# Optimization experiments

Measured on AMD Instinct MI355X. Metric: run time of the kernel, lower is better.

The kernel has to match this reference:

```python
import jax, jax.numpy as jnp
import numpy as np

K = 8192
D = 256


def setup_inputs() -> dict:
    key = jax.random.key(0)
    k1, k2 = jax.random.split(key)
    z_e_x = jax.random.normal(k1, (8, D, 1024), dtype=jnp.float32)  # (B, D, T)
    # nn.Embedding(K, D) weight init: uniform(-1/K, 1/K)
    codebook = jax.random.uniform(k2, (K, D), dtype=jnp.float32,
                                  minval=-1.0 / K, maxval=1.0 / K)
    return {"z_e_x": z_e_x, "codebook": codebook}


def reference(z_e_x, codebook):
    # z_e_x: (B, D, T) -> (B, T, D), matching z_e_x.permute(0, 2, 1)
    z = jnp.transpose(z_e_x, (0, 2, 1))  # (B, T, D)
    # squared L2 distance: ||z||^2 + ||e||^2 - 2 z @ e^T
    z_sq = jnp.sum(z * z, axis=-1, keepdims=True)            # (B, T, 1)
    e_sq = jnp.sum(codebook * codebook, axis=-1)             # (K,)
    cross = jnp.einsum('btd,kd->btk', z, codebook)           # (B, T, K)
    dists = z_sq + e_sq[None, None, :] - 2.0 * cross         # (B, T, K)
    indices = jnp.argmin(dists, axis=-1)                     # (B, T) int
    return indices
```

## Files before the change

kernel.cpp:

```cpp
#include <hip/hip_runtime.h>
#include <cfloat>
#include <stdint.h>

#define KC 8192
#define NQ 8192
#define DD 256
#define NSTAGE 8

typedef _Float16 f16;
typedef _Float16 half8 __attribute__((ext_vector_type(8)));
typedef float floatx4 __attribute__((ext_vector_type(4)));

#define WS_AH   0
#define WS_AL   4194304
#define WS_BH   8388608
#define WS_BL1  12582912
#define WS_KEY1 16777216
#define WS_NEED1 (16777216ull + 65536ull)
#define WS_BL2  10485760
#define WS_KEY2 12582912

__device__ __forceinline__ void prep_b_body(const float* __restrict__ cb,
                                            f16* __restrict__ Bh, f16* __restrict__ Bl,
                                            int kofs, int gid) {
    int n = gid & 127;
    int q = (gid >> 7) & 3;
    int s = (gid >> 9) & 7;
    int ntl = gid >> 12;
    int K = kofs + ntl * 128 + n;
    int d0 = s * 32 + q * 8;
    const float4 v0 = *(const float4*)(cb + (size_t)K * DD + d0);
    const float4 v1 = *(const float4*)(cb + (size_t)K * DD + d0 + 4);
    float vv[8] = {v0.x, v0.y, v0.z, v0.w, v1.x, v1.y, v1.z, v1.w};
    half8 eh8, el8;
    #pragma unroll
    for (int j = 0; j < 8; ++j) {
        float e = vv[j] * 8192.0f;
        f16 h = (f16)e;
        eh8[j] = h;
        el8[j] = (f16)(e - (float)h);
    }
    *(half8*)(Bh + (size_t)gid * 8) = eh8;
    *(half8*)(Bl + (size_t)gid * 8) = el8;
}

__device__ __forceinline__ void prep_a_vec_body(const float* __restrict__ z,
                                                f16* __restrict__ Ah, f16* __restrict__ Al,
                                                int bid, int tid) {
    const int mt = bid >> 3;
    const int s  = bid & 7;
    const int q  = tid >> 6;
    const int lane = tid & 63;
    const int r0 = lane * 4;
    const int Q0 = mt * 256;
    const int b = Q0 >> 10;
    const int t0 = (Q0 & 1023) + r0;
    const float* zp = z + (size_t)b * (DD * 1024) + t0;
    const int d0 = s * 32 + q * 8;
    float4 v[8];
    #pragma unroll
    for (int j = 0; j < 8; ++j)
        v[j] = *(const float4*)(zp + (size_t)(d0 + j) * 1024);
    const size_t gbase = (((size_t)(mt * 8 + s) * 4 + q) * 256 + r0);
    #pragma unroll
    for (int dq = 0; dq < 4; ++dq) {
        half8 zh8, zl8;
        #pragma unroll
        for (int j = 0; j < 8; ++j) {
            float vv = (dq == 0) ? v[j].x : (dq == 1) ? v[j].y : (dq == 2) ? v[j].z : v[j].w;
            f16 h = (f16)vv;
            zh8[j] = h;
            zl8[j] = (f16)(vv - (float)h);
        }
        *(half8*)(Ah + (gbase + dq) * 8) = zh8;
        *(half8*)(Al + (gbase + dq) * 8) = zl8;
    }
}

__device__ __forceinline__ void zsq2_body(const float* __restrict__ z,
                                          float* __restrict__ zsq,
                                          unsigned long long* __restrict__ key,
                                          int gid) {
    int q = gid >> 1, half = gid & 1;
    int b = q >> 10, t = q & 1023;
    const float* p = z + (size_t)b * (DD * 1024) + t + (size_t)(half * 128) * 1024;
    float s = 0.f;
    #pragma unroll 8
    for (int d = 0; d < 128; ++d) { float v = p[(size_t)d * 1024]; s = fmaf(v, v, s); }
    float so = __shfl_xor(s, 1, 64);
    if (half == 0) { zsq[q] = s + so; key[q] = ~0ull; }
}

__global__ void vq_prep_all(const float* __restrict__ z, const float* __restrict__ cb,
                            f16* __restrict__ Ah, f16* __restrict__ Al,
                            f16* __restrict__ Bh, f16* __restrict__ Bl,
                            float* __restrict__ zsq, unsigned long long* __restrict__ key) {
    int bid = blockIdx.x;
    int tid = threadIdx.x;
    if (bid < 64) {
        zsq2_body(z, zsq, key, bid * 256 + tid);
    } else if (bid < 320) {
        prep_a_vec_body(z, Ah, Al, bid - 64, tid);
    } else {
        prep_b_body(cb, Bh, Bl, 0, (bid - 320) * 256 + tid);
    }
}

__global__ void vq_prep_az(const float* __restrict__ z,
                           f16* __restrict__ Ah, f16* __restrict__ Al,
                           float* __restrict__ zsq, unsigned long long* __restrict__ key) {
    int bid = blockIdx.x;
    if (bid < 64) zsq2_body(z, zsq, key, bid * 256 + threadIdx.x);
    else          prep_a_vec_body(z, Ah, Al, bid - 64, threadIdx.x);
}
__global__ void vq_prep_b(const float* __restrict__ cb,
                          f16* __restrict__ Bh, f16* __restrict__ Bl, int kofs) {
    prep_b_body(cb, Bh, Bl, kofs, blockIdx.x * 256 + threadIdx.x);
}

__global__ __launch_bounds__(256, 4)
void vq_gemm16(const f16* __restrict__ Ah, const f16* __restrict__ Al,
               const f16* __restrict__ Bh, const f16* __restrict__ Bl,
               const float* __restrict__ zsq, unsigned long long* __restrict__ keyp,
               int kofs) {
    const int flat = blockIdx.x;
    const int xcd = flat & 7;
    const int idx = flat >> 3;
    const int mh2 = xcd * 8 + ((idx >> 3) & 7);
    const int ntl = (idx >> 6) * 8 + (idx & 7);
    const int tid = threadIdx.x;
    const int lane = tid & 63;
    const int wv = tid >> 6;
    const int wm = wv >> 1, wn = wv & 1;
    const int quad = lane >> 4;
    const int l16 = lane & 15;

    __shared__ unsigned long long kbuf[256];

    floatx4 acc[4][4];
    #pragma unroll
    for (int i = 0; i < 4; ++i)
        #pragma unroll
        for (int j = 0; j < 4; ++j) acc[i][j] = (floatx4)0.f;

    const int mt = mh2 >> 1;
    const int r0 = (mh2 & 1) * 128;
    const size_t abase = ((((size_t)(mt * 8) * 4) + quad) * 256
                          + (size_t)(r0 + wm * 64 + l16)) * 8;
    const f16* Ap  = Ah + abase;
    const f16* Alp = Al + abase;
    const f16* Bpb = Bh + ((size_t)(ntl * 8) * 4 + quad) * 1024 + (size_t)(wn * 64 + l16) * 8;
    const f16* Blb = Bl + ((size_t)(ntl * 8) * 4 + quad) * 1024 + (size_t)(wn * 64 + l16) * 8;

    for (int s = 0; s < NSTAGE; ++s) {
        half8 bhf[4], blf[4];
        #pragma unroll
        for (int nj = 0; nj < 4; ++nj) {
            bhf[nj] = *(const half8*)(Bpb + nj * 128);
            blf[nj] = *(const half8*)(Blb + nj * 128);
        }
        half8 av[4], aw[4];
        #pragma unroll
        for (int mi = 0; mi < 4; ++mi) {
            av[mi] = *(const half8*)(Ap  + (size_t)mi * 128);
            aw[mi] = *(const half8*)(Alp + (size_t)mi * 128);
        }
        #pragma unroll
        for (int mi = 0; mi < 4; ++mi)
            #pragma unroll
            for (int nj = 0; nj < 4; ++nj)
                acc[mi][nj] = __builtin_amdgcn_mfma_f32_16x16x32_f16(av[mi], bhf[nj], acc[mi][nj], 0, 0, 0);
        #pragma unroll
        for (int mi = 0; mi < 4; ++mi)
            #pragma unroll
            for (int nj = 0; nj < 4; ++nj)
                acc[mi][nj] = __builtin_amdgcn_mfma_f32_16x16x32_f16(av[mi], blf[nj], acc[mi][nj], 0, 0, 0);
        #pragma unroll
        for (int mi = 0; mi < 4; ++mi)
            #pragma unroll
            for (int nj = 0; nj < 4; ++nj)
                acc[mi][nj] = __builtin_amdgcn_mfma_f32_16x16x32_f16(aw[mi], bhf[nj], acc[mi][nj], 0, 0, 0);
        Ap  += 8192; Alp += 8192;
        Bpb += 4096; Blb += 4096;
    }

    const int kb = kofs + ntl * 128 + wn * 64;
    #pragma unroll
    for (int mi = 0; mi < 4; ++mi) {
        #pragma unroll
        for (int reg = 0; reg < 4; ++reg) {
            int qlocal = wm * 64 + mi * 16 + quad * 4 + reg;
            float zq = zsq[mh2 * 128 + qlocal];
            float bd = FLT_MAX; int bk = 0;
            #pragma unroll
            for (int nj = 0; nj < 4; ++nj) {
                float dd = zq - acc[mi][nj][reg] * 0x1p-12f;
                int kk = kb + nj * 16 + l16;
                if (dd < bd || (dd == bd && kk < bk)) { bd = dd; bk = kk; }
            }
            #pragma unroll
            for (int mm = 1; mm <= 8; mm <<= 1) {
                float od = __shfl_xor(bd, mm, 64);
                int ok = __shfl_xor(bk, mm, 64);
                if (od < bd || (od == bd && ok < bk)) { bd = od; bk = ok; }
            }
            if (l16 == 0)
                kbuf[wn * 128 + qlocal] =
                    ((unsigned long long)__float_as_uint(bd) << 32) | (unsigned int)bk;
        }
    }
    __syncthreads();
    if (tid < 128) {
        unsigned long long k0 = kbuf[tid];
        unsigned long long k1 = kbuf[128 + tid];
        unsigned long long key = (k1 < k0) ? k1 : k0;
        atomicMin(&keyp[mh2 * 128 + tid], key);
    }
}

__global__ void vq_extract(const unsigned long long* __restrict__ key,
                           int* __restrict__ out) {
    int q = blockIdx.x * 256 + threadIdx.x;
    out[q] = (int)(key[q] & 0xFFFFFFFFull);
}

extern "C" void kernel_launch(void* const* d_in, const int* in_sizes, int n_in,
                              void* d_out, int out_size, void* d_ws, size_t ws_size,
                              hipStream_t stream) {
    const float* z  = (const float*)d_in[0];
    const float* cb = (const float*)d_in[1];
    char* ws = (char*)d_ws;
    f16* Ah = (f16*)(ws + WS_AH);
    f16* Al = (f16*)(ws + WS_AL);
    float* zsq = (float*)d_out;
    int* out = (int*)d_out;

    if (ws_size >= WS_NEED1) {
        f16* Bh = (f16*)(ws + WS_BH);
        f16* Bl = (f16*)(ws + WS_BL1);
        unsigned long long* key = (unsigned long long*)(ws + WS_KEY1);
        vq_prep_all<<<1344, 256, 0, stream>>>(z, cb, Ah, Al, Bh, Bl, zsq, key);
        vq_gemm16<<<4096, 256, 0, stream>>>(Ah, Al, Bh, Bl, zsq, key, 0);
        vq_extract<<<NQ / 256, 256, 0, stream>>>(key, out);
    } else {
        f16* Bh = (f16*)(ws + WS_BH);
        f16* Bl = (f16*)(ws + WS_BL2);
        unsigned long long* key = (unsigned long long*)(ws + WS_KEY2);
        vq_prep_az<<<320, 256, 0, stream>>>(z, Ah, Al, zsq, key);
        for (int p = 0; p < 2; ++p) {
            int kofs = p * 4096;
            vq_prep_b<<<512, 256, 0, stream>>>(cb, Bh, Bl, kofs);
            vq_gemm16<<<2048, 256, 0, stream>>>(Ah, Al, Bh, Bl, zsq, key, kofs);
        }
        vq_extract<<<NQ / 256, 256, 0, stream>>>(key, out);
    }
}
```

Before: 187.9 us.

## Switch GEMM from 16x16x32 to 32x32x16 MFMA with matching operand layout

Replaces the 16x16x32 f16 MFMA tiling (4x4 accumulators per wave) with 32x32x16 MFMA (2x2 floatx16 accumulators). The A and B prep kernels now write a permuted K-chunk layout so each half-wave loads contiguous half8 fragments in the order the 32x32 instruction expects. The epilogue argmin reduction is reworked for the 32-lane output pattern. The aim is higher MFMA throughput and fewer operand loads per FLOP. The risk is a layout or index mismatch, since the permutation, pointer strides and row mapping must all agree.

```diff
diff --git a/kernel.cpp b/kernel.cpp
--- a/kernel.cpp
+++ b/kernel.cpp
@@ -9,7 +9,7 @@
 
 typedef _Float16 f16;
 typedef _Float16 half8 __attribute__((ext_vector_type(8)));
-typedef float floatx4 __attribute__((ext_vector_type(4)));
+typedef float floatx16 __attribute__((ext_vector_type(16)));
 
 #define WS_AH   0
 #define WS_AL   4194304
@@ -40,8 +40,10 @@
         eh8[j] = h;
         el8[j] = (f16)(e - (float)h);
     }
-    *(half8*)(Bh + (size_t)gid * 8) = eh8;
-    *(half8*)(Bl + (size_t)gid * 8) = el8;
+    int sig = ((q & 1) << 1) | (q >> 1);
+    size_t og = ((size_t)(ntl * 8 + s) * 4 + sig) * 128 + n;
+    *(half8*)(Bh + og * 8) = eh8;
+    *(half8*)(Bl + og * 8) = el8;
 }
 
 __device__ __forceinline__ void prep_a_vec_body(const float* __restrict__ z,
@@ -61,7 +63,9 @@
     #pragma unroll
     for (int j = 0; j < 8; ++j)
         v[j] = *(const float4*)(zp + (size_t)(d0 + j) * 1024);
-    const size_t gbase = (((size_t)(mt * 8 + s) * 4 + q) * 256 + r0);
+    const int sig = ((q & 1) << 1) | (q >> 1);
+    const int mh2 = mt * 2 + (r0 >> 7);
+    const size_t gbase = ((size_t)(mh2 * 8 + s) * 4 + sig) * 128 + (r0 & 127);
     #pragma unroll
     for (int dq = 0; dq < 4; ++dq) {
         half8 zh8, zl8;
@@ -119,7 +123,7 @@
 }
 
 __global__ __launch_bounds__(256, 4)
-void vq_gemm16(const f16* __restrict__ Ah, const f16* __restrict__ Al,
+void vq_gemm32(const f16* __restrict__ Ah, const f16* __restrict__ Al,
                const f16* __restrict__ Bh, const f16* __restrict__ Bl,
                const float* __restrict__ zsq, unsigned long long* __restrict__ keyp,
                int kofs) {
@@ -132,79 +136,85 @@
     const int lane = tid & 63;
     const int wv = tid >> 6;
     const int wm = wv >> 1, wn = wv & 1;
-    const int quad = lane >> 4;
-    const int l16 = lane & 15;
+    const int hi = lane >> 5;
+    const int l32 = lane & 31;
 
     __shared__ unsigned long long kbuf[256];
 
-    floatx4 acc[4][4];
-    #pragma unroll
-    for (int i = 0; i < 4; ++i)
-        #pragma unroll
-        for (int j = 0; j < 4; ++j) acc[i][j] = (floatx4)0.f;
-
-    const int mt = mh2 >> 1;
-    const int r0 = (mh2 & 1) * 128;
-    const size_t abase = ((((size_t)(mt * 8) * 4) + quad) * 256
-                          + (size_t)(r0 + wm * 64 + l16)) * 8;
-    const f16* Ap  = Ah + abase;
-    const f16* Alp = Al + abase;
-    const f16* Bpb = Bh + ((size_t)(ntl * 8) * 4 + quad) * 1024 + (size_t)(wn * 64 + l16) * 8;
-    const f16* Blb = Bl + ((size_t)(ntl * 8) * 4 + quad) * 1024 + (size_t)(wn * 64 + l16) * 8;
+    floatx16 acc[2][2];
+    #pragma unroll
+    for (int i = 0; i < 2; ++i)
+        #pragma unroll
+        for (int j = 0; j < 2; ++j) acc[i][j] = (floatx16)0.f;
+
+    const f16* Ap  = Ah + ((size_t)(mh2 * 32 + 2 * hi)) * 1024
+                        + (size_t)(wm * 64 + l32) * 8;
+    const f16* Alp = Al + ((size_t)(mh2 * 32 + 2 * hi)) * 1024
+                        + (size_t)(wm * 64 + l32) * 8;
+    const f16* Bpb = Bh + ((size_t)(ntl * 32 + 2 * hi)) * 1024
+                        + (size_t)(wn * 64 + l32) * 8;
+    const f16* Blb = Bl + ((size_t)(ntl * 32 + 2 * hi)) * 1024
+                        + (size_t)(wn * 64 + l32) * 8;
 
     for (int s = 0; s < NSTAGE; ++s) {
-        half8 bhf[4], blf[4];
-        #pragma unroll
-        for (int nj = 0; nj < 4; ++nj) {
-            bhf[nj] = *(const half8*)(Bpb + nj * 128);
-            blf[nj] = *(const half8*)(Blb + nj * 128);
-        }
-        half8 av[4], aw[4];
-        #pragma unroll
-        for (int mi = 0; mi < 4; ++mi) {
-            av[mi] = *(const half8*)(Ap  + (size_t)mi * 128);
-            aw[mi] = *(const half8*)(Alp + (size_t)mi * 128);
-        }
-        #pragma unroll
-        for (int mi = 0; mi < 4; ++mi)
-            #pragma unroll
-            for (int nj = 0; nj < 4; ++nj)
-                acc[mi][nj] = __builtin_amdgcn_mfma_f32_16x16x32_f16(av[mi], bhf[nj], acc[mi][nj], 0, 0, 0);
-        #pragma unroll
-        for (int mi = 0; mi < 4; ++mi)
-            #pragma unroll
-            for (int nj = 0; nj < 4; ++nj)
-                acc[mi][nj] = __builtin_amdgcn_mfma_f32_16x16x32_f16(av[mi], blf[nj], acc[mi][nj], 0, 0, 0);
-        #pragma unroll
-        for (int mi = 0; mi < 4; ++mi)
-            #pragma unroll
-            for (int nj = 0; nj < 4; ++nj)
-                acc[mi][nj] = __builtin_amdgcn_mfma_f32_16x16x32_f16(aw[mi], bhf[nj], acc[mi][nj], 0, 0, 0);
-        Ap  += 8192; Alp += 8192;
-        Bpb += 4096; Blb += 4096;
+        half8 a0[2][2], a1[2][2], b0[2][2], b1[2][2];
+        #pragma unroll
+        for (int t = 0; t < 2; ++t)
+            #pragma unroll
+            for (int i = 0; i < 2; ++i) {
+                a0[t][i] = *(const half8*)(Ap  + t * 1024 + i * 256);
+                a1[t][i] = *(const half8*)(Alp + t * 1024 + i * 256);
+                b0[t][i] = *(const half8*)(Bpb + t * 1024 + i * 256);
+                b1[t][i] = *(const half8*)(Blb + t * 1024 + i * 256);
+            }
+        #pragma unroll
+        for (int t = 0; t < 2; ++t)
+            #pragma unroll
+            for (int mi = 0; mi < 2; ++mi)
+                #pragma unroll
+                for (int nj = 0; nj < 2; ++nj)
+                    acc[mi][nj] = __builtin_amdgcn_mfma_f32_32x32x16_f16(
+                        a0[t][mi], b0[t][nj], acc[mi][nj], 0, 0, 0);
+        #pragma unroll
+        for (int t = 0; t < 2; ++t)
+            #pragma unroll
+            for (int mi = 0; mi < 2; ++mi)
+                #pragma unroll
+                for (int nj = 0; nj < 2; ++nj)
+                    acc[mi][nj] = __builtin_amdgcn_mfma_f32_32x32x16_f16(
+                        a0[t][mi], b1[t][nj], acc[mi][nj], 0, 0, 0);
+        #pragma unroll
+        for (int t = 0; t < 2; ++t)
+            #pragma unroll
+            for (int mi = 0; mi < 2; ++mi)
+                #pragma unroll
+                for (int nj = 0; nj < 2; ++nj)
+                    acc[mi][nj] = __builtin_amdgcn_mfma_f32_32x32x16_f16(
+                        a1[t][mi], b0[t][nj], acc[mi][nj], 0, 0, 0);
+        Ap += 4096; Alp += 4096; Bpb += 4096; Blb += 4096;
     }
 
     const int kb = kofs + ntl * 128 + wn * 64;
     #pragma unroll
-    for (int mi = 0; mi < 4; ++mi) {
-        #pragma unroll
-        for (int reg = 0; reg < 4; ++reg) {
-            int qlocal = wm * 64 + mi * 16 + quad * 4 + reg;
+    for (int mi = 0; mi < 2; ++mi) {
+        #pragma unroll
+        for (int reg = 0; reg < 16; ++reg) {
+            int qlocal = wm * 64 + mi * 32 + (reg & 3) + 8 * (reg >> 2) + 4 * hi;
             float zq = zsq[mh2 * 128 + qlocal];
             float bd = FLT_MAX; int bk = 0;
             #pragma unroll
-            for (int nj = 0; nj < 4; ++nj) {
+            for (int nj = 0; nj < 2; ++nj) {
                 float dd = zq - acc[mi][nj][reg] * 0x1p-12f;
-                int kk = kb + nj * 16 + l16;
+                int kk = kb + nj * 32 + l32;
                 if (dd < bd || (dd == bd && kk < bk)) { bd = dd; bk = kk; }
             }
             #pragma unroll
-            for (int mm = 1; mm <= 8; mm <<= 1) {
+            for (int mm = 1; mm <= 16; mm <<= 1) {
                 float od = __shfl_xor(bd, mm, 64);
                 int ok = __shfl_xor(bk, mm, 64);
                 if (od < bd || (od == bd && ok < bk)) { bd = od; bk = ok; }
             }
-            if (l16 == 0)
+            if (l32 == 0)
                 kbuf[wn * 128 + qlocal] =
                     ((unsigned long long)__float_as_uint(bd) << 32) | (unsigned int)bk;
         }
@@ -240,7 +250,7 @@
         f16* Bl = (f16*)(ws + WS_BL1);
         unsigned long long* key = (unsigned long long*)(ws + WS_KEY1);
         vq_prep_all<<<1344, 256, 0, stream>>>(z, cb, Ah, Al, Bh, Bl, zsq, key);
-        vq_gemm16<<<4096, 256, 0, stream>>>(Ah, Al, Bh, Bl, zsq, key, 0);
+        vq_gemm32<<<4096, 256, 0, stream>>>(Ah, Al, Bh, Bl, zsq, key, 0);
         vq_extract<<<NQ / 256, 256, 0, stream>>>(key, out);
     } else {
         f16* Bh = (f16*)(ws + WS_BH);
@@ -250,7 +260,7 @@
         for (int p = 0; p < 2; ++p) {
             int kofs = p * 4096;
             vq_prep_b<<<512, 256, 0, stream>>>(cb, Bh, Bl, kofs);
-            vq_gemm16<<<2048, 256, 0, stream>>>(Ah, Al, Bh, Bl, zsq, key, kofs);
+            vq_gemm32<<<2048, 256, 0, stream>>>(Ah, Al, Bh, Bl, zsq, key, kofs);
         }
         vq_extract<<<NQ / 256, 256, 0, stream>>>(key, out);
     }
```

New measurement: 228.0 us. +21.4%, slower.

## Software-pipeline fragment loads across K-stages with register double buffering

Applied to the files above, without the earlier changes.

Replaces the per-stage load-then-compute loop with a manually unrolled schedule. Global loads of the next stage's A/B hi/lo fragments are issued between MFMA groups so that memory latency overlaps with matrix math, and the fragment registers are rotated between stages. This keeps the same three products per stage (Ah*Bh, Ah*Bl, Al*Bh) in a reordered sequence. It holds more fragments live at once, which raises register pressure under the 4-block occupancy bound.

```diff
diff --git a/kernel.cpp b/kernel.cpp
--- a/kernel.cpp
+++ b/kernel.cpp
@@ -117,6 +117,13 @@
                           f16* __restrict__ Bh, f16* __restrict__ Bl, int kofs) {
     prep_b_body(cb, Bh, Bl, kofs, blockIdx.x * 256 + threadIdx.x);
 }
+
+#define TERM16(AF, BF) do {                                                     \
+    _Pragma("unroll") for (int _m = 0; _m < 4; ++_m)                            \
+      _Pragma("unroll") for (int _n = 0; _n < 4; ++_n)                          \
+        acc[_m][_n] = __builtin_amdgcn_mfma_f32_16x16x32_f16(                   \
+            AF[_m], BF[_n], acc[_m][_n], 0, 0, 0);                              \
+} while (0)
 
 __global__ __launch_bounds__(256, 4)
 void vq_gemm16(const f16* __restrict__ Ah, const f16* __restrict__ Al,
@@ -152,36 +159,48 @@
     const f16* Bpb = Bh + ((size_t)(ntl * 8) * 4 + quad) * 1024 + (size_t)(wn * 64 + l16) * 8;
     const f16* Blb = Bl + ((size_t)(ntl * 8) * 4 + quad) * 1024 + (size_t)(wn * 64 + l16) * 8;
 
-    for (int s = 0; s < NSTAGE; ++s) {
-        half8 bhf[4], blf[4];
-        #pragma unroll
-        for (int nj = 0; nj < 4; ++nj) {
-            bhf[nj] = *(const half8*)(Bpb + nj * 128);
-            blf[nj] = *(const half8*)(Blb + nj * 128);
-        }
-        half8 av[4], aw[4];
-        #pragma unroll
-        for (int mi = 0; mi < 4; ++mi) {
-            av[mi] = *(const half8*)(Ap  + (size_t)mi * 128);
-            aw[mi] = *(const half8*)(Alp + (size_t)mi * 128);
-        }
-        #pragma unroll
-        for (int mi = 0; mi < 4; ++mi)
-            #pragma unroll
-            for (int nj = 0; nj < 4; ++nj)
-                acc[mi][nj] = __builtin_amdgcn_mfma_f32_16x16x32_f16(av[mi], bhf[nj], acc[mi][nj], 0, 0, 0);
-        #pragma unroll
-        for (int mi = 0; mi < 4; ++mi)
-            #pragma unroll
-            for (int nj = 0; nj < 4; ++nj)
-                acc[mi][nj] = __builtin_amdgcn_mfma_f32_16x16x32_f16(av[mi], blf[nj], acc[mi][nj], 0, 0, 0);
-        #pragma unroll
-        for (int mi = 0; mi < 4; ++mi)
-            #pragma unroll
-            for (int nj = 0; nj < 4; ++nj)
-                acc[mi][nj] = __builtin_amdgcn_mfma_f32_16x16x32_f16(aw[mi], bhf[nj], acc[mi][nj], 0, 0, 0);
-        Ap  += 8192; Alp += 8192;
-        Bpb += 4096; Blb += 4096;
+    half8 A0[4], A1[4], B0[4], B1[4];
+    #pragma unroll
+    for (int i = 0; i < 4; ++i) {
+        A0[i] = *(const half8*)(Ap  + (size_t)i * 128);
+        A1[i] = *(const half8*)(Alp + (size_t)i * 128);
+        B0[i] = *(const half8*)(Bpb + i * 128);
+        B1[i] = *(const half8*)(Blb + i * 128);
+    }
+
+    #pragma unroll
+    for (int su = 0; su < 4; ++su) {
+        TERM16(A0, B0);
+        TERM16(A1, B0);
+        #pragma unroll
+        for (int i = 0; i < 4; ++i) {
+            A1[i] = *(const half8*)(Ap  + 8192 + (size_t)i * 128);
+            B0[i] = *(const half8*)(Bpb + 4096 + i * 128);
+        }
+        TERM16(A0, B1);
+        #pragma unroll
+        for (int i = 0; i < 4; ++i) {
+            A0[i] = *(const half8*)(Alp + 8192 + (size_t)i * 128);
+            B1[i] = *(const half8*)(Blb + 4096 + i * 128);
+        }
+        TERM16(A1, B0);
+        TERM16(A0, B0);
+        if (su < 3) {
+            #pragma unroll
+            for (int i = 0; i < 4; ++i) {
+                A0[i] = *(const half8*)(Ap  + 16384 + (size_t)i * 128);
+                B0[i] = *(const half8*)(Bpb + 8192 + i * 128);
+            }
+        }
+        TERM16(A1, B1);
+        if (su < 3) {
+            #pragma unroll
+            for (int i = 0; i < 4; ++i) {
+                A1[i] = *(const half8*)(Alp + 16384 + (size_t)i * 128);
+                B1[i] = *(const half8*)(Blb + 8192 + i * 128);
+            }
+            Ap += 16384; Alp += 16384; Bpb += 8192; Blb += 8192;
+        }
     }
 
     const int kb = kofs + ntl * 128 + wn * 64;
```

After: 186.3 us. No clear change (-0.9%).
